# Optimization experiments

Hardware: AMD Instinct MI355X
Metric: run time of the kernel (lower is better)

## Reference

```python
import jax, jax.numpy as jnp
import numpy as np

BATCH = 32
NUM_VARS = 16
SAMPLES = 4096
EMBED_DIM = 128
WINDOW_SIZE = 32
STEP_SIZE = 4
WIDTH = 1.0


def setup_inputs() -> dict:
    key = jax.random.key(0)
    k1, k2, k3, k4, k5 = jax.random.split(key, 5)
    x = jax.random.normal(k1, (BATCH, NUM_VARS, SAMPLES), dtype=jnp.float32)
    # sample-level LSH: num_variables -> embed_dim
    W_sample = jax.random.normal(k2, (NUM_VARS, EMBED_DIM), dtype=jnp.float32)
    b_sample = jax.random.uniform(k3, (EMBED_DIM,), dtype=jnp.float32, minval=0.0, maxval=WIDTH)
    # patch-level LSH: window_size*embed_dim -> embed_dim
    W_patch = jax.random.normal(k4, (WINDOW_SIZE * EMBED_DIM, EMBED_DIM), dtype=jnp.float32)
    b_patch = jax.random.uniform(k5, (EMBED_DIM,), dtype=jnp.float32, minval=0.0, maxval=WIDTH)
    return {"x": x, "W_sample": W_sample, "b_sample": b_sample,
            "W_patch": W_patch, "b_patch": b_patch}


def reference(x, W_sample, b_sample, W_patch, b_patch):
    batch, v, samples = x.shape
    # encode: E2LSH hash of every timestep, fully vectorized over the samples axis
    # enc: [B, S, D]
    enc = jnp.floor((jnp.einsum('bvs,vd->bsd', x, W_sample) + b_sample) / WIDTH)
    # quantize: sliding windows over time, flattened then hashed
    num_tokens = (samples - WINDOW_SIZE) // STEP_SIZE  # matches preallocated tokens
    # idx: [T, W] gather indices for all windows at once
    idx = jnp.arange(num_tokens)[:, None] * STEP_SIZE + jnp.arange(WINDOW_SIZE)[None, :]
    windows = enc[:, idx, :].reshape(batch, num_tokens, WINDOW_SIZE * EMBED_DIM)  # [B, T, W*D]
    tokens = jnp.floor((windows @ W_patch + b_patch) / WIDTH)  # [B, T, D]
    return tokens
```

## Files before the change

### kernel.cpp

```cpp
#include <hip/hip_runtime.h>
#include <hip/hip_bf16.h>
#include <cstdint>

#define BATCH   32
#define NVARS   16
#define SAMPLES 4096
#define EDIM    128
#define NTOK    1016
#define KDIM    4096

typedef __bf16 bf8_t __attribute__((ext_vector_type(8)));
typedef float  f4_t  __attribute__((ext_vector_type(4)));

__device__ __forceinline__ void gload_lds16(const void* g, void* l) {
  __builtin_amdgcn_global_load_lds(
      (const __attribute__((address_space(1))) unsigned int*)g,
      (__attribute__((address_space(3))) unsigned int*)l, 16, 0, 0);
}

__global__ __launch_bounds__(256) void prep_kernel(
    const float* __restrict__ x, const float* __restrict__ Ws,
    const float* __restrict__ bs, const float* __restrict__ Wp,
    __hip_bfloat16* __restrict__ enc, __hip_bfloat16* __restrict__ WtF)
{
  __shared__ float smem[32 * 132];
  int tid = threadIdx.x;

  if (blockIdx.x < 512) {
    float (*xs)[256] = (float(*)[256])smem;
    int b  = blockIdx.x >> 4;
    int s0 = (blockIdx.x & 15) << 8;
    int u0 = s0 >> 2;

    {
      int col = (tid & 63) << 2;
      int v0  = tid >> 6;
#pragma unroll
      for (int j = 0; j < 4; ++j) {
        int v = v0 + j * 4;
        float4 t = *(const float4*)(x + (size_t)b * NVARS * SAMPLES
                                    + (size_t)v * SAMPLES + s0 + col);
        *(float4*)&xs[v][col] = t;
      }
    }

    int wv = tid >> 6, lane = tid & 63;
    int rlane = lane >> 2, c = lane & 3;
    int e = wv;
    int d0 = e * 32 + c * 8;

    float w[NVARS][8];
#pragma unroll
    for (int v = 0; v < NVARS; ++v) {
      float4 w0 = *(const float4*)&Ws[v * EDIM + d0];
      float4 w1 = *(const float4*)&Ws[v * EDIM + d0 + 4];
      w[v][0] = w0.x; w[v][1] = w0.y; w[v][2] = w0.z; w[v][3] = w0.w;
      w[v][4] = w1.x; w[v][5] = w1.y; w[v][6] = w1.z; w[v][7] = w1.w;
    }
    float bias[8];
    {
      float4 b0 = *(const float4*)&bs[d0];
      float4 b1 = *(const float4*)&bs[d0 + 4];
      bias[0] = b0.x; bias[1] = b0.y; bias[2] = b0.z; bias[3] = b0.w;
      bias[4] = b1.x; bias[5] = b1.y; bias[6] = b1.z; bias[7] = b1.w;
    }

    __syncthreads();

#pragma unroll
    for (int p = 0; p < 4; ++p)
#pragma unroll
      for (int uc = 0; uc < 4; ++uc) {
        int ur   = uc * 16 + rlane;
        int sloc = 4 * ur + p;
        float acc[8];
#pragma unroll
        for (int j = 0; j < 8; ++j) acc[j] = bias[j];
#pragma unroll
        for (int v = 0; v < NVARS; ++v) {
          float xv = xs[v][sloc];
#pragma unroll
          for (int j = 0; j < 8; ++j) acc[j] += xv * w[v][j];
        }
        union { unsigned short u[8]; uint4 q; } pk;
#pragma unroll
        for (int j = 0; j < 8; ++j)
          pk.u[j] = (unsigned short)(__float_as_uint(floorf(acc[j])) >> 16);
        int u    = u0 + ur;
        int phys = (c + (u >> 1)) & 3;
        size_t off = (((size_t)b * 4 + p) * 4 + e) * 32768 + (size_t)u * 32
                   + phys * 8;
        *(uint4*)(enc + off) = pk.q;
      }
  } else {
    float (*ls)[132] = (float(*)[132])smem;
    int kb  = blockIdx.x - 512;
    int s   = kb >> 3, dlt = kb & 7;
    int kbase = (4 * dlt + (s & 3)) * 128 + (s >> 2) * 32;
#pragma unroll
    for (int r = 0; r < 16; ++r) {
      int idx = tid + r * 256;
      ls[idx >> 7][idx & 127] =
          Wp[(size_t)(kbase + (idx >> 7)) * EDIM + (idx & 127)];
    }
    __syncthreads();
    int g = tid >> 5, l5 = tid & 31;
#pragma unroll
    for (int h = 0; h < 2; ++h) {
      int lane = l5 + h * 32;
      int quad = lane >> 4, l15 = lane & 15;
      int n = g * 16 + l15;
      union { unsigned short u[8]; uint4 v; } pk;
#pragma unroll
      for (int t = 0; t < 8; ++t) {
        __hip_bfloat16 hh = __float2bfloat16(ls[quad * 8 + t][n]);
        pk.u[t] = *(unsigned short*)&hh;
      }
      *(uint4*)(WtF + (size_t)kb * 4096 + g * 512 + lane * 8) = pk.v;
    }
  }
}

__global__ __launch_bounds__(512, 2) void gemm_kernel(
    const __hip_bfloat16* __restrict__ enc,
    const __hip_bfloat16* __restrict__ WtF,
    const float* __restrict__ bp,
    float* __restrict__ out)
{
  __shared__ __align__(16) __hip_bfloat16 Apl[2][2][4608];

  int tid  = threadIdx.x;
  int lane = tid & 63;
  int wv   = tid >> 6;
  int g    = wv >> 2;
  int wq   = wv & 3;
  int b    = blockIdx.x >> 3;
  int t0   = (blockIdx.x & 7) << 7;
  int wm   = (wq >> 1) << 6;
  int wn   = (wq & 1) << 6;
  int quad = lane >> 4;
  int l15  = lane & 15;

  const __hip_bfloat16* encb = enc + (size_t)b * 524288;
  const __hip_bfloat16* bg   = WtF + (size_t)(wn >> 4) * 512 + lane * 8;

  f4_t acc[4][4];
  f4_t zero = {0.f, 0.f, 0.f, 0.f};
#pragma unroll
  for (int i = 0; i < 4; ++i)
#pragma unroll
    for (int j = 0; j < 4; ++j) acc[i][j] = zero;

  auto stageA = [&](int sp, int buf) {
    const __hip_bfloat16* gp = encb
        + (size_t)((sp & 3) * 4 + (sp >> 2)) * 32768
        + (size_t)t0 * 32 + lane * 8;
    __hip_bfloat16* dst = &Apl[g][buf][0];
    int u3 = (wq == 0) ? 8 : (wq * 2 + 1);
    gload_lds16(gp + (size_t)(wq * 2) * 512,     dst + (wq * 2) * 512);
    gload_lds16(gp + (size_t)(wq * 2 + 1) * 512, dst + (wq * 2 + 1) * 512);
    gload_lds16(gp + (size_t)u3 * 512,           dst + u3 * 512);
  };

  auto loadB = [&](int kb, uint4* d) {
#pragma unroll
    for (int j = 0; j < 4; ++j)
      d[j] = *(const uint4*)(bg + (size_t)kb * 4096 + j * 512);
  };

  auto compute = [&](int abuf, int dlt, const uint4* bq) {
    const bf8_t* pA = (const bf8_t*)&Apl[g][abuf][0];
    int swzA = (quad + ((t0 + dlt + wm + l15) >> 1)) & 3;
    bf8_t af[4];
#pragma unroll
    for (int i = 0; i < 4; ++i)
      af[i] = pA[(dlt + wm + i * 16 + l15) * 4 + swzA];
#pragma unroll
    for (int mi = 0; mi < 4; ++mi)
#pragma unroll
      for (int ni = 0; ni < 4; ++ni)
        acc[mi][ni] = __builtin_amdgcn_mfma_f32_16x16x32_bf16(
            af[mi], __builtin_bit_cast(bf8_t, bq[ni]), acc[mi][ni], 0, 0, 0);
  };

  stageA(g * 8, 0);
  asm volatile("s_waitcnt vmcnt(0)" ::: "memory");
  asm volatile("s_barrier" ::: "memory");

  uint4 bq[2][4];
  loadB(g * 64, bq[0]);
  loadB(g * 64 + 1, bq[1]);

  for (int ss = 0; ss < 8; ++ss) {
    if (ss < 7) stageA(g * 8 + ss + 1, (ss + 1) & 1);
#pragma unroll
    for (int d = 0; d < 8; ++d) {
      int kl = ss * 8 + d;
      compute(ss & 1, d, bq[d & 1]);
      if (kl < 62) loadB(g * 64 + kl + 2, bq[d & 1]);
    }
    asm volatile("s_barrier" ::: "memory");
  }

  float* rb = (float*)&Apl[0][0][0];
  int widx = (wq * 64 + lane) * 17;
  float bias[4];
#pragma unroll
  for (int ni = 0; ni < 4; ++ni) bias[ni] = bp[wn + ni * 16 + l15];

#pragma unroll
  for (int mi = 0; mi < 4; ++mi) {
    __syncthreads();
    if (g == 1) {
#pragma unroll
      for (int ni = 0; ni < 4; ++ni)
#pragma unroll
        for (int r = 0; r < 4; ++r)
          rb[widx + ni * 4 + r] = acc[mi][ni][r];
    }
    __syncthreads();
    if (g == 0) {
#pragma unroll
      for (int ni = 0; ni < 4; ++ni)
#pragma unroll
        for (int r = 0; r < 4; ++r) {
          int t = t0 + wm + mi * 16 + quad * 4 + r;
          if (t < NTOK) {
            int n = wn + ni * 16 + l15;
            out[((size_t)b * NTOK + t) * EDIM + n] =
                floorf(acc[mi][ni][r] + rb[widx + ni * 4 + r] + bias[ni]);
          }
        }
    }
  }
}

extern "C" void kernel_launch(void* const* d_in, const int* in_sizes, int n_in,
                              void* d_out, int out_size, void* d_ws, size_t ws_size,
                              hipStream_t stream) {
  const float* x  = (const float*)d_in[0];
  const float* Ws = (const float*)d_in[1];
  const float* bs = (const float*)d_in[2];
  const float* Wp = (const float*)d_in[3];
  const float* bp = (const float*)d_in[4];
  float* out = (float*)d_out;

  __hip_bfloat16* enc = (__hip_bfloat16*)d_ws;
  __hip_bfloat16* WtF = (__hip_bfloat16*)((char*)d_ws +
                        (size_t)BATCH * SAMPLES * EDIM * sizeof(__hip_bfloat16));

  prep_kernel<<<512 + 128, 256, 0, stream>>>(x, Ws, bs, Wp, enc, WtF);
  gemm_kernel<<<BATCH * 8, 512, 0, stream>>>(enc, WtF, bp, out);
}
```

Before: 121.6 us.

## Fuse sample-level encoding into GEMM kernel, computing A tiles on the fly

Removes the global bf16 encoding buffer. The GEMM kernel now loads raw x into LDS, transposed, and computes the floor-hashed sample embedding directly into the A staging buffers, interleaved with the MFMA loop. The prep kernel keeps only the W_patch bf16 repack. The aim is to cut the global write and read-back of the 32 MB encoding tensor, at the cost of redundant encoding work across overlapping windows, more registers and extra LDS. MFMA sections are also wrapped with s_setprio to favour matrix issue.

```diff
diff --git a/kernel.cpp b/kernel.cpp
--- a/kernel.cpp
+++ b/kernel.cpp
@@ -7,127 +7,51 @@
 #define SAMPLES 4096
 #define EDIM    128
 #define NTOK    1016
-#define KDIM    4096
 
 typedef __bf16 bf8_t __attribute__((ext_vector_type(8)));
 typedef float  f4_t  __attribute__((ext_vector_type(4)));
 
-__device__ __forceinline__ void gload_lds16(const void* g, void* l) {
-  __builtin_amdgcn_global_load_lds(
-      (const __attribute__((address_space(1))) unsigned int*)g,
-      (__attribute__((address_space(3))) unsigned int*)l, 16, 0, 0);
+__global__ __launch_bounds__(256) void prep_kernel(
+    const float* __restrict__ Wp, __hip_bfloat16* __restrict__ WtF)
+{
+  __shared__ float ls[32][132];
+  int tid = threadIdx.x;
+  int kb  = blockIdx.x;
+  int s = kb >> 3, dlt = kb & 7;
+  int kbase = (4 * dlt + (s & 3)) * 128 + (s >> 2) * 32;
+#pragma unroll
+  for (int r = 0; r < 16; ++r) {
+    int idx = tid + r * 256;
+    ls[idx >> 7][idx & 127] =
+        Wp[(size_t)(kbase + (idx >> 7)) * EDIM + (idx & 127)];
+  }
+  __syncthreads();
+  int g = tid >> 5, l5 = tid & 31;
+#pragma unroll
+  for (int h = 0; h < 2; ++h) {
+    int lane = l5 + h * 32;
+    int quad = lane >> 4, l15 = lane & 15;
+    int n = g * 16 + l15;
+    union { unsigned short u[8]; uint4 v; } pk;
+#pragma unroll
+    for (int t = 0; t < 8; ++t) {
+      __hip_bfloat16 hh = __float2bfloat16(ls[quad * 8 + t][n]);
+      pk.u[t] = *(unsigned short*)&hh;
+    }
+    *(uint4*)(WtF + (size_t)kb * 4096 + g * 512 + lane * 8) = pk.v;
+  }
 }
 
-__global__ __launch_bounds__(256) void prep_kernel(
-    const float* __restrict__ x, const float* __restrict__ Ws,
-    const float* __restrict__ bs, const float* __restrict__ Wp,
-    __hip_bfloat16* __restrict__ enc, __hip_bfloat16* __restrict__ WtF)
-{
-  __shared__ float smem[32 * 132];
-  int tid = threadIdx.x;
-
-  if (blockIdx.x < 512) {
-    float (*xs)[256] = (float(*)[256])smem;
-    int b  = blockIdx.x >> 4;
-    int s0 = (blockIdx.x & 15) << 8;
-    int u0 = s0 >> 2;
-
-    {
-      int col = (tid & 63) << 2;
-      int v0  = tid >> 6;
-#pragma unroll
-      for (int j = 0; j < 4; ++j) {
-        int v = v0 + j * 4;
-        float4 t = *(const float4*)(x + (size_t)b * NVARS * SAMPLES
-                                    + (size_t)v * SAMPLES + s0 + col);
-        *(float4*)&xs[v][col] = t;
-      }
-    }
-
-    int wv = tid >> 6, lane = tid & 63;
-    int rlane = lane >> 2, c = lane & 3;
-    int e = wv;
-    int d0 = e * 32 + c * 8;
-
-    float w[NVARS][8];
-#pragma unroll
-    for (int v = 0; v < NVARS; ++v) {
-      float4 w0 = *(const float4*)&Ws[v * EDIM + d0];
-      float4 w1 = *(const float4*)&Ws[v * EDIM + d0 + 4];
-      w[v][0] = w0.x; w[v][1] = w0.y; w[v][2] = w0.z; w[v][3] = w0.w;
-      w[v][4] = w1.x; w[v][5] = w1.y; w[v][6] = w1.z; w[v][7] = w1.w;
-    }
-    float bias[8];
-    {
-      float4 b0 = *(const float4*)&bs[d0];
-      float4 b1 = *(const float4*)&bs[d0 + 4];
-      bias[0] = b0.x; bias[1] = b0.y; bias[2] = b0.z; bias[3] = b0.w;
-      bias[4] = b1.x; bias[5] = b1.y; bias[6] = b1.z; bias[7] = b1.w;
-    }
-
-    __syncthreads();
-
-#pragma unroll
-    for (int p = 0; p < 4; ++p)
-#pragma unroll
-      for (int uc = 0; uc < 4; ++uc) {
-        int ur   = uc * 16 + rlane;
-        int sloc = 4 * ur + p;
-        float acc[8];
-#pragma unroll
-        for (int j = 0; j < 8; ++j) acc[j] = bias[j];
-#pragma unroll
-        for (int v = 0; v < NVARS; ++v) {
-          float xv = xs[v][sloc];
-#pragma unroll
-          for (int j = 0; j < 8; ++j) acc[j] += xv * w[v][j];
-        }
-        union { unsigned short u[8]; uint4 q; } pk;
-#pragma unroll
-        for (int j = 0; j < 8; ++j)
-          pk.u[j] = (unsigned short)(__float_as_uint(floorf(acc[j])) >> 16);
-        int u    = u0 + ur;
-        int phys = (c + (u >> 1)) & 3;
-        size_t off = (((size_t)b * 4 + p) * 4 + e) * 32768 + (size_t)u * 32
-                   + phys * 8;
-        *(uint4*)(enc + off) = pk.q;
-      }
-  } else {
-    float (*ls)[132] = (float(*)[132])smem;
-    int kb  = blockIdx.x - 512;
-    int s   = kb >> 3, dlt = kb & 7;
-    int kbase = (4 * dlt + (s & 3)) * 128 + (s >> 2) * 32;
-#pragma unroll
-    for (int r = 0; r < 16; ++r) {
-      int idx = tid + r * 256;
-      ls[idx >> 7][idx & 127] =
-          Wp[(size_t)(kbase + (idx >> 7)) * EDIM + (idx & 127)];
-    }
-    __syncthreads();
-    int g = tid >> 5, l5 = tid & 31;
-#pragma unroll
-    for (int h = 0; h < 2; ++h) {
-      int lane = l5 + h * 32;
-      int quad = lane >> 4, l15 = lane & 15;
-      int n = g * 16 + l15;
-      union { unsigned short u[8]; uint4 v; } pk;
-#pragma unroll
-      for (int t = 0; t < 8; ++t) {
-        __hip_bfloat16 hh = __float2bfloat16(ls[quad * 8 + t][n]);
-        pk.u[t] = *(unsigned short*)&hh;
-      }
-      *(uint4*)(WtF + (size_t)kb * 4096 + g * 512 + lane * 8) = pk.v;
-    }
-  }
-}
-
 __global__ __launch_bounds__(512, 2) void gemm_kernel(
-    const __hip_bfloat16* __restrict__ enc,
+    const float* __restrict__ x,
+    const float* __restrict__ Ws,
+    const float* __restrict__ bs,
     const __hip_bfloat16* __restrict__ WtF,
     const float* __restrict__ bp,
     float* __restrict__ out)
 {
   __shared__ __align__(16) __hip_bfloat16 Apl[2][2][4608];
+  __shared__ __align__(16) float xT[4][136][20];
 
   int tid  = threadIdx.x;
   int lane = tid & 63;
@@ -141,8 +65,7 @@
   int quad = lane >> 4;
   int l15  = lane & 15;
 
-  const __hip_bfloat16* encb = enc + (size_t)b * 524288;
-  const __hip_bfloat16* bg   = WtF + (size_t)(wn >> 4) * 512 + lane * 8;
+  const __hip_bfloat16* bg = WtF + (size_t)(wn >> 4) * 512 + lane * 8;
 
   f4_t acc[4][4];
   f4_t zero = {0.f, 0.f, 0.f, 0.f};
@@ -151,15 +74,57 @@
 #pragma unroll
     for (int j = 0; j < 4; ++j) acc[i][j] = zero;
 
-  auto stageA = [&](int sp, int buf) {
-    const __hip_bfloat16* gp = encb
-        + (size_t)((sp & 3) * 4 + (sp >> 2)) * 32768
-        + (size_t)t0 * 32 + lane * 8;
-    __hip_bfloat16* dst = &Apl[g][buf][0];
-    int u3 = (wq == 0) ? 8 : (wq * 2 + 1);
-    gload_lds16(gp + (size_t)(wq * 2) * 512,     dst + (wq * 2) * 512);
-    gload_lds16(gp + (size_t)(wq * 2 + 1) * 512, dst + (wq * 2 + 1) * 512);
-    gload_lds16(gp + (size_t)u3 * 512,           dst + u3 * 512);
+  {
+    int v = tid >> 5, l5 = tid & 31;
+    const float* xb = x + ((size_t)b * NVARS + v) * SAMPLES;
+    int sb = t0 << 2;
+#pragma unroll
+    for (int j = 0; j < 17; ++j) {
+      int i = l5 + j * 32;
+      int s = sb + i; s = s > (SAMPLES - 1) ? (SAMPLES - 1) : s;
+      xT[i & 3][i >> 2][v] = xb[s];
+    }
+  }
+
+  float w[NVARS][4];
+  float bz[4];
+  auto loadW = [&](int e) {
+    int d0 = e * 32 + (tid & 7) * 4;
+#pragma unroll
+    for (int v = 0; v < NVARS; ++v)
+      *(float4*)&w[v][0] = *(const float4*)(Ws + v * EDIM + d0);
+    *(float4*)&bz[0] = *(const float4*)(bs + d0);
+  };
+  loadW(g * 2);
+
+  auto encU = [&](int Pg, int buf, int k) {
+    int gt = tid & 255;
+    if (k == 4 && gt >= 64) return;
+    int p  = Pg & 3;
+    int r0 = gt >> 3;
+    int r  = (k < 4) ? (r0 + k * 32) : (128 + r0);
+    int h  = tid & 7;
+    const float* xrow = &xT[p][r][0];
+    float xr[NVARS];
+    *(float4*)&xr[0]  = *(const float4*)(xrow + 0);
+    *(float4*)&xr[4]  = *(const float4*)(xrow + 4);
+    *(float4*)&xr[8]  = *(const float4*)(xrow + 8);
+    *(float4*)&xr[12] = *(const float4*)(xrow + 12);
+    float a0 = bz[0], a1 = bz[1], a2 = bz[2], a3 = bz[3];
+#pragma unroll
+    for (int v = 0; v < NVARS; ++v) {
+      a0 += xr[v] * w[v][0]; a1 += xr[v] * w[v][1];
+      a2 += xr[v] * w[v][2]; a3 += xr[v] * w[v][3];
+    }
+    int u    = t0 + r;
+    int phys = ((h >> 1) + (u >> 1)) & 3;
+    union { unsigned short us[4]; uint2 q; } pk;
+    pk.us[0] = (unsigned short)(__float_as_uint(floorf(a0)) >> 16);
+    pk.us[1] = (unsigned short)(__float_as_uint(floorf(a1)) >> 16);
+    pk.us[2] = (unsigned short)(__float_as_uint(floorf(a2)) >> 16);
+    pk.us[3] = (unsigned short)(__float_as_uint(floorf(a3)) >> 16);
+    *(uint2*)(&Apl[g][buf][0] + (size_t)r * 32 + phys * 8 + (h & 1) * 4) =
+        pk.q;
   };
 
   auto loadB = [&](int kb, uint4* d) {
@@ -168,23 +133,27 @@
       d[j] = *(const uint4*)(bg + (size_t)kb * 4096 + j * 512);
   };
 
-  auto compute = [&](int abuf, int dlt, const uint4* bq) {
+  auto compute = [&](int abuf, int dlt, const uint4* bq_) {
     const bf8_t* pA = (const bf8_t*)&Apl[g][abuf][0];
     int swzA = (quad + ((t0 + dlt + wm + l15) >> 1)) & 3;
     bf8_t af[4];
 #pragma unroll
     for (int i = 0; i < 4; ++i)
       af[i] = pA[(dlt + wm + i * 16 + l15) * 4 + swzA];
+    __builtin_amdgcn_s_setprio(1);
 #pragma unroll
     for (int mi = 0; mi < 4; ++mi)
 #pragma unroll
       for (int ni = 0; ni < 4; ++ni)
         acc[mi][ni] = __builtin_amdgcn_mfma_f32_16x16x32_bf16(
-            af[mi], __builtin_bit_cast(bf8_t, bq[ni]), acc[mi][ni], 0, 0, 0);
-  };
-
-  stageA(g * 8, 0);
-  asm volatile("s_waitcnt vmcnt(0)" ::: "memory");
+            af[mi], __builtin_bit_cast(bf8_t, bq_[ni]), acc[mi][ni], 0, 0, 0);
+    __builtin_amdgcn_s_setprio(0);
+  };
+
+  __syncthreads();
+#pragma unroll
+  for (int k = 0; k < 5; ++k) encU(g * 8, 0, k);
+  asm volatile("s_waitcnt lgkmcnt(0)" ::: "memory");
   asm volatile("s_barrier" ::: "memory");
 
   uint4 bq[2][4];
@@ -192,13 +161,15 @@
   loadB(g * 64 + 1, bq[1]);
 
   for (int ss = 0; ss < 8; ++ss) {
-    if (ss < 7) stageA(g * 8 + ss + 1, (ss + 1) & 1);
+    if (ss == 3) loadW(g * 2 + 1);
 #pragma unroll
     for (int d = 0; d < 8; ++d) {
       int kl = ss * 8 + d;
       compute(ss & 1, d, bq[d & 1]);
       if (kl < 62) loadB(g * 64 + kl + 2, bq[d & 1]);
-    }
+      if (ss < 7 && d < 5) encU(g * 8 + ss + 1, (ss + 1) & 1, d);
+    }
+    asm volatile("s_waitcnt lgkmcnt(0)" ::: "memory");
     asm volatile("s_barrier" ::: "memory");
   }
 
@@ -245,10 +216,8 @@
   const float* bp = (const float*)d_in[4];
   float* out = (float*)d_out;
 
-  __hip_bfloat16* enc = (__hip_bfloat16*)d_ws;
-  __hip_bfloat16* WtF = (__hip_bfloat16*)((char*)d_ws +
-                        (size_t)BATCH * SAMPLES * EDIM * sizeof(__hip_bfloat16));
-
-  prep_kernel<<<512 + 128, 256, 0, stream>>>(x, Ws, bs, Wp, enc, WtF);
-  gemm_kernel<<<BATCH * 8, 512, 0, stream>>>(enc, WtF, bp, out);
+  __hip_bfloat16* WtF = (__hip_bfloat16*)d_ws;
+
+  prep_kernel<<<128, 256, 0, stream>>>(Wp, WtF);
+  gemm_kernel<<<BATCH * 8, 512, 0, stream>>>(x, Ws, bs, WtF, bp, out);
 }
```

Result: slower. 125.0 us (+2.8%).
